# Optimization experiments

Hardware: AMD Instinct MI355X
Metric: run time of the kernel (lower is better)

The kernel has to match this reference:

```python
import jax, jax.numpy as jnp
import numpy as np

B, H, P, K, E, BN = 8, 256, 1024, 32, 4, 64


def setup_inputs() -> dict:
    key = jax.random.key(0)
    ks = jax.random.split(key, 8)
    current = jax.random.normal(ks[0], (B, H, P), dtype=jnp.float32)
    neighbor_features = jax.random.normal(ks[1], (B, H, P, K), dtype=jnp.float32)
    # binary {0,1} validity mask, stored as float like the torch module expects
    neighbor_validity = jax.random.randint(ks[2], (B, 1, P, K), 0, 2).astype(jnp.float32)
    edge_features = jax.random.normal(ks[3], (B, E, P, K), dtype=jnp.float32)
    # 1x1 Conv2d weights flattened to matrices: (out_ch, in_ch)
    w1 = jax.random.normal(ks[4], (BN, 2 * H + E), dtype=jnp.float32) * 0.05
    b1 = jnp.zeros((BN,), dtype=jnp.float32)
    w2 = jax.random.normal(ks[5], (BN,), dtype=jnp.float32) * 0.05  # second conv: out_ch=1
    b2 = jnp.zeros((), dtype=jnp.float32)
    return {
        "current": current,
        "neighbor_features": neighbor_features,
        "neighbor_validity": neighbor_validity,
        "edge_features": edge_features,
        "w1": w1,
        "b1": b1,
        "w2": w2,
        "b2": b2,
    }


def reference(current, neighbor_features, neighbor_validity, edge_features, w1, b1, w2, b2):
    h_dim = current.shape[1]
    # Split the 1x1-conv weight along the concat axis so we never materialize
    # the [B, 2H+E, P, K] concatenated tensor (same math as cat + conv1x1).
    w1c = w1[:, :h_dim]            # acts on broadcast center features
    w1n = w1[:, h_dim:2 * h_dim]   # acts on neighbor features
    w1e = w1[:, 2 * h_dim:]        # acts on edge features

    hid = (
        jnp.einsum("bcp,oc->bop", current, w1c)[:, :, :, None]
        + jnp.einsum("bcpk,oc->bopk", neighbor_features, w1n)
        + jnp.einsum("bcpk,oc->bopk", edge_features, w1e)
        + b1[None, :, None, None]
    )
    hid = jax.nn.relu(hid)                                  # (B, BN, P, K)
    logits = jnp.einsum("bopk,o->bpk", hid, w2) + b2        # (B, P, K)

    valid = neighbor_validity[:, 0] > 0.5                   # (B, P, K) bool
    logits = jnp.where(valid, logits, -jnp.inf)
    has_any = jnp.any(valid, axis=-1, keepdims=True)        # (B, P, 1)
    logits_safe = jnp.where(has_any, logits, 0.0)           # all-masked rows -> 0 logits
    weights = jax.nn.softmax(logits_safe, axis=-1)
    weights = jnp.where(has_any & valid, weights, 0.0)      # zero weight on pads / empty rows

    pooled = jnp.einsum("bcpk,bpk->bcp", neighbor_features, weights)
    return pooled
```

## Files before the change

### kernel.cpp

```cpp
#include <hip/hip_runtime.h>
#include <math.h>


#define B_ 8
#define H_ 256
#define P_ 1024
#define K_ 32
#define E_ 4
#define BN_ 64

typedef __attribute__((ext_vector_type(8))) short short8;
typedef __attribute__((ext_vector_type(4))) float floatx4;

__device__ __forceinline__ unsigned short bf16_rne(float f) {
  unsigned u = __float_as_uint(f);
  u += 0x7fffu + ((u >> 16) & 1u);
  return (unsigned short)(u >> 16);
}
__device__ __forceinline__ unsigned pack_bf16_rne(float lo, float hi) {
  unsigned u0 = __float_as_uint(lo);
  u0 += 0x7fffu + ((u0 >> 16) & 1u);
  unsigned u1 = __float_as_uint(hi);
  u1 += 0x7fffu + ((u1 >> 16) & 1u);
  return (u0 >> 16) | (u1 & 0xffff0000u);
}

__global__ __launch_bounds__(256) void prep_kernel(
    const float* __restrict__ w1, unsigned short* __restrict__ w1m) {
  int i = blockIdx.x * 256 + threadIdx.x;
  if (i >= 4 * 17 * 64 * 8) return;
  int j = i & 7, lane = (i >> 3) & 63;
  int kt = i >> 9;
  int mt = kt / 17, ki = kt % 17;
  int o = mt * 16 + (lane & 15);
  int c = ki * 32 + (lane >> 4) * 8 + j;
  float v = (c < 516) ? w1[o * 516 + c] : 0.f;
  w1m[i] = bf16_rne(v);
}

__global__ __launch_bounds__(256, 4) void soft_attn_agg_kernel(
    const float* __restrict__ cur,
    const float* __restrict__ nf,
    const float* __restrict__ nv,
    const float* __restrict__ ef,
    const unsigned short* __restrict__ w1m,
    const float* __restrict__ b1,
    const float* __restrict__ w2,
    float* __restrict__ out) {
  __shared__ unsigned s_nf_dw[BN_ * 132];
  __shared__ __align__(16) unsigned short s_curb[2][H_];
  __shared__ __align__(16) unsigned short s_edgeT[2][K_][8];
  __shared__ float s_valid[64];
  __shared__ __align__(16) float s_b1[BN_];
  __shared__ __align__(16) float s_w2[BN_];
  __shared__ float s_lg[BN_];
  __shared__ float s_wt[64];

  const int t = threadIdx.x;
  const unsigned bid = blockIdx.x;
  const unsigned xcd = bid & 7u, sidx = bid >> 3;
  const int p0 = (int)(2u * (xcd * 64u + (sidx & 63u)));
  const int b = (int)(sidx >> 6);

  const int w = t >> 6;
  const int lane = t & 63;
  const int q = lane >> 4;
  const int ln15 = lane & 15;

  {
    const int r = lane >> 4, s = lane & 15;
    const float* base = nf + ((size_t)b * H_ * P_ + (size_t)p0) * K_;
    const int X = (s & 14) << 1;
    unsigned* dst0 = s_nf_dw + (4 * s) * 132;
#pragma unroll
    for (int i = 0; i < 8; ++i) {
      const int c_even = w * 64 + i * 8 + 2 * r;
      const float4 fa = *(const float4*)(base + (size_t)c_even * (P_ * K_) + s * 4);
      const float4 fb = *(const float4*)(base + (size_t)(c_even + 1) * (P_ * K_) + s * 4);
      const int cp = (32 * w + 4 * i + r) ^ X;
      unsigned* dst = dst0 + cp;
      dst[0]   = pack_bf16_rne(fa.x, fb.x);
      dst[132] = pack_bf16_rne(fa.y, fb.y);
      dst[264] = pack_bf16_rne(fa.z, fb.z);
      dst[396] = pack_bf16_rne(fa.w, fb.w);
    }
  }
  {
    const float* cp_ = cur + ((size_t)b * H_ + t) * P_ + p0;
    s_curb[0][t] = bf16_rne(cp_[0]);
    s_curb[1][t] = bf16_rne(cp_[1]);
  }
  if (t < 64) {
    s_valid[t] = nv[((size_t)b * P_ + p0) * K_ + t];
    const int pl = t >> 5, k = t & 31;
    const float* ep = ef + (((size_t)b * E_ * P_) + p0 + pl) * K_ + k;
    float e0 = ep[0];
    float e1 = ep[(size_t)P_ * K_];
    float e2 = ep[(size_t)(2 * P_) * K_];
    float e3 = ep[(size_t)(3 * P_) * K_];
    uint4 d;
    d.x = pack_bf16_rne(e0, e1);
    d.y = pack_bf16_rne(e2, e3);
    d.z = 0u; d.w = 0u;
    *(uint4*)&s_edgeT[pl][k][0] = d;
  } else if (t < 128) {
    s_b1[t - 64] = b1[t - 64];
  } else if (t < 192) {
    s_w2[t - 128] = w2[t - 128];
  }
  __syncthreads();

  floatx4 acc[4];
#pragma unroll
  for (int mt = 0; mt < 4; ++mt)
    acc[mt] = *(const floatx4*)&s_b1[mt * 16 + q * 4];

  const int pl_w = w >> 1;
  const int n_lane = 16 * w + ln15;
  const int bxor = ((2 * w + (ln15 >> 3)) & 7) << 2;
  const unsigned* bsrc = s_nf_dw + n_lane * 132;
  const unsigned short* w1m_l = w1m + (size_t)lane * 8;

#pragma unroll
  for (int ki = 0; ki < 17; ++ki) {
    short8 bfrag;
    if (ki < 8) {
      bfrag = *(const short8*)&s_curb[pl_w][ki * 32 + q * 8];
    } else if (ki < 16) {
      bfrag = *(const short8*)(bsrc + ((16 * (ki - 8) + 4 * q) ^ bxor));
    } else {
      bfrag = *(const short8*)&s_edgeT[pl_w][(w & 1) * 16 + ln15][0];
    }
#pragma unroll
    for (int mt = 0; mt < 4; ++mt) {
      short8 a = *(const short8*)(w1m_l + (size_t)(mt * 17 + ki) * 512);
      acc[mt] = __builtin_amdgcn_mfma_f32_16x16x32_bf16(a, bfrag, acc[mt], 0, 0, 0);
    }
  }

  {
    float lp = 0.f;
#pragma unroll
    for (int mt = 0; mt < 4; ++mt) {
      const floatx4 w2v = *(const floatx4*)&s_w2[mt * 16 + q * 4];
#pragma unroll
      for (int r = 0; r < 4; ++r)
        lp = fmaf(fmaxf(acc[mt][r], 0.f), w2v[r], lp);
    }
    lp += __shfl_xor(lp, 16);
    lp += __shfl_xor(lp, 32);
    if (lane < 16) s_lg[16 * w + lane] = lp;
  }
  __syncthreads();

  if (t < 64) {
    float lg = s_lg[t];
    bool v = s_valid[t] > 0.5f;
    float ml = v ? lg : -INFINITY;
#pragma unroll
    for (int m = 1; m < 32; m <<= 1) ml = fmaxf(ml, __shfl_xor(ml, m));
    float e = v ? __expf(lg - ml) : 0.f;
    float ssum = e;
#pragma unroll
    for (int m = 1; m < 32; m <<= 1) ssum += __shfl_xor(ssum, m);
    s_wt[t] = (ml > -INFINITY) ? (e / ssum) : 0.f;
  }
  __syncthreads();

  {
    const int pl = t >> 7, cpair = t & 127;
    float acc0 = 0.f, acc1 = 0.f;
#pragma unroll
    for (int k = 0; k < K_; ++k) {
      const int n = pl * 32 + k;
      const int xr = ((n >> 3) & 7) << 2;
      const unsigned u = s_nf_dw[n * 132 + (cpair ^ xr)];
      const float wtk = s_wt[n];
      acc0 = fmaf(__uint_as_float(u << 16), wtk, acc0);
      acc1 = fmaf(__uint_as_float(u & 0xffff0000u), wtk, acc1);
    }
    float* op = out + ((size_t)b * H_ + 2 * cpair) * P_ + p0 + pl;
    op[0] = acc0;
    op[P_] = acc1;
  }
}

extern "C" void kernel_launch(void* const* d_in, const int* in_sizes, int n_in,
                              void* d_out, int out_size, void* d_ws,
                              size_t ws_size, hipStream_t stream) {
  const float* cur = (const float*)d_in[0];
  const float* nf  = (const float*)d_in[1];
  const float* nv  = (const float*)d_in[2];
  const float* ef  = (const float*)d_in[3];
  const float* w1  = (const float*)d_in[4];
  const float* b1  = (const float*)d_in[5];
  const float* w2  = (const float*)d_in[6];

  unsigned short* w1m = (unsigned short*)d_ws;
  prep_kernel<<<(4 * 17 * 64 * 8 + 255) / 256, 256, 0, stream>>>(w1, w1m);
  soft_attn_agg_kernel<<<B_ * P_ / 2, 256, 0, stream>>>(
      cur, nf, nv, ef, w1m, b1, w2, (float*)d_out);
}
```

Before: 417.5 us.

## Process eight points per 512-thread block with coalesced neighbor loads

Each block now covers eight points with eight waves instead of two points with four waves. Neighbor features are staged by having each thread read one contiguous neighbor element across many channels, which gives coalesced global loads, and the XOR swizzle in shared memory is dropped. Each wave computes two neighbor tiles for one point, so every weight fragment feeds two MFMAs, and the output is written as float2. The shared-memory footprint grows to about 135KB, so only one block fits per CU, which reduces latency hiding, and the unswizzled layout may cause more LDS bank conflicts.

```diff
diff --git a/kernel.cpp b/kernel.cpp
--- a/kernel.cpp
+++ b/kernel.cpp
@@ -38,7 +38,7 @@
   w1m[i] = bf16_rne(v);
 }
 
-__global__ __launch_bounds__(256, 4) void soft_attn_agg_kernel(
+__global__ __launch_bounds__(512, 2) void soft_attn_agg_kernel(
     const float* __restrict__ cur,
     const float* __restrict__ nf,
     const float* __restrict__ nv,
@@ -47,20 +47,21 @@
     const float* __restrict__ b1,
     const float* __restrict__ w2,
     float* __restrict__ out) {
-  __shared__ unsigned s_nf_dw[BN_ * 132];
-  __shared__ __align__(16) unsigned short s_curb[2][H_];
-  __shared__ __align__(16) unsigned short s_edgeT[2][K_][8];
-  __shared__ float s_valid[64];
-  __shared__ __align__(16) float s_b1[BN_];
-  __shared__ __align__(16) float s_w2[BN_];
-  __shared__ float s_lg[BN_];
-  __shared__ float s_wt[64];
+  __shared__ unsigned s_nf[256 * 132];
+  __shared__ unsigned short s_curb[8][264];
+  __shared__ unsigned s_edge[8][32][4];
+  __shared__ float s_valid[256];
+  __shared__ float s_b1v[BN_];
+  __shared__ float s_w2v[BN_];
+  __shared__ float s_lg[256];
+  __shared__ float s_wt[256];
 
   const int t = threadIdx.x;
   const unsigned bid = blockIdx.x;
-  const unsigned xcd = bid & 7u, sidx = bid >> 3;
-  const int p0 = (int)(2u * (xcd * 64u + (sidx & 63u)));
-  const int b = (int)(sidx >> 6);
+  const unsigned xcd = bid & 7u, sx = bid >> 3;
+  const int b = (int)(sx >> 4);
+  const int pg = (int)(xcd * 16u + (sx & 15u));
+  const int p0 = pg * 8;
 
   const int w = t >> 6;
   const int lane = t & 63;
@@ -68,92 +69,120 @@
   const int ln15 = lane & 15;
 
   {
-    const int r = lane >> 4, s = lane & 15;
-    const float* base = nf + ((size_t)b * H_ * P_ + (size_t)p0) * K_;
-    const int X = (s & 14) << 1;
-    unsigned* dst0 = s_nf_dw + (4 * s) * 132;
-#pragma unroll
-    for (int i = 0; i < 8; ++i) {
-      const int c_even = w * 64 + i * 8 + 2 * r;
-      const float4 fa = *(const float4*)(base + (size_t)c_even * (P_ * K_) + s * 4);
-      const float4 fb = *(const float4*)(base + (size_t)(c_even + 1) * (P_ * K_) + s * 4);
-      const int cp = (32 * w + 4 * i + r) ^ X;
-      unsigned* dst = dst0 + cp;
-      dst[0]   = pack_bf16_rne(fa.x, fb.x);
-      dst[132] = pack_bf16_rne(fa.y, fb.y);
-      dst[264] = pack_bf16_rne(fa.z, fb.z);
-      dst[396] = pack_bf16_rne(fa.w, fb.w);
-    }
-  }
-  {
-    const float* cp_ = cur + ((size_t)b * H_ + t) * P_ + p0;
-    s_curb[0][t] = bf16_rne(cp_[0]);
-    s_curb[1][t] = bf16_rne(cp_[1]);
-  }
-  if (t < 64) {
+    const int n = t & 255, ch = t >> 8;
+    const float* gp = nf + (size_t)b * (H_ * P_ * K_) +
+                      (size_t)(ch * 128) * (P_ * K_) + (size_t)p0 * K_ + n;
+    unsigned* drow = s_nf + n * 132 + ch * 64;
+#pragma unroll 4
+    for (int i = 0; i < 16; ++i) {
+      const float* gc = gp + (size_t)(8 * i) * (P_ * K_);
+      float f0 = gc[0];
+      float f1 = gc[(size_t)(P_ * K_)];
+      float f2 = gc[(size_t)(2 * P_ * K_)];
+      float f3 = gc[(size_t)(3 * P_ * K_)];
+      float f4 = gc[(size_t)(4 * P_ * K_)];
+      float f5 = gc[(size_t)(5 * P_ * K_)];
+      float f6 = gc[(size_t)(6 * P_ * K_)];
+      float f7 = gc[(size_t)(7 * P_ * K_)];
+      uint4 d;
+      d.x = pack_bf16_rne(f0, f1);
+      d.y = pack_bf16_rne(f2, f3);
+      d.z = pack_bf16_rne(f4, f5);
+      d.w = pack_bf16_rne(f6, f7);
+      *(uint4*)&drow[4 * i] = d;
+    }
+  }
+  if (t < 256) {
+    const float* cb = cur + ((size_t)b * H_ + t) * P_ + p0;
+    float4 ca = *(const float4*)cb;
+    float4 cc = *(const float4*)(cb + 4);
+    s_curb[0][t] = bf16_rne(ca.x);
+    s_curb[1][t] = bf16_rne(ca.y);
+    s_curb[2][t] = bf16_rne(ca.z);
+    s_curb[3][t] = bf16_rne(ca.w);
+    s_curb[4][t] = bf16_rne(cc.x);
+    s_curb[5][t] = bf16_rne(cc.y);
+    s_curb[6][t] = bf16_rne(cc.z);
+    s_curb[7][t] = bf16_rne(cc.w);
     s_valid[t] = nv[((size_t)b * P_ + p0) * K_ + t];
     const int pl = t >> 5, k = t & 31;
-    const float* ep = ef + (((size_t)b * E_ * P_) + p0 + pl) * K_ + k;
+    const float* ep = ef + (size_t)b * (E_ * P_ * K_) + (size_t)p0 * K_ + t;
     float e0 = ep[0];
-    float e1 = ep[(size_t)P_ * K_];
-    float e2 = ep[(size_t)(2 * P_) * K_];
-    float e3 = ep[(size_t)(3 * P_) * K_];
+    float e1 = ep[(size_t)(P_ * K_)];
+    float e2 = ep[(size_t)(2 * P_ * K_)];
+    float e3 = ep[(size_t)(3 * P_ * K_)];
     uint4 d;
     d.x = pack_bf16_rne(e0, e1);
     d.y = pack_bf16_rne(e2, e3);
-    d.z = 0u; d.w = 0u;
-    *(uint4*)&s_edgeT[pl][k][0] = d;
-  } else if (t < 128) {
-    s_b1[t - 64] = b1[t - 64];
-  } else if (t < 192) {
-    s_w2[t - 128] = w2[t - 128];
+    d.z = 0u;
+    d.w = 0u;
+    *(uint4*)&s_edge[pl][k][0] = d;
+  } else if (t < 320) {
+    s_b1v[t - 256] = b1[t - 256];
+  } else if (t < 384) {
+    s_w2v[t - 320] = w2[t - 320];
   }
   __syncthreads();
 
-  floatx4 acc[4];
-#pragma unroll
-  for (int mt = 0; mt < 4; ++mt)
-    acc[mt] = *(const floatx4*)&s_b1[mt * 16 + q * 4];
-
-  const int pl_w = w >> 1;
-  const int n_lane = 16 * w + ln15;
-  const int bxor = ((2 * w + (ln15 >> 3)) & 7) << 2;
-  const unsigned* bsrc = s_nf_dw + n_lane * 132;
+  floatx4 acc[4][2];
+#pragma unroll
+  for (int mt = 0; mt < 4; ++mt) {
+    floatx4 binit = *(const floatx4*)&s_b1v[mt * 16 + q * 4];
+    acc[mt][0] = binit;
+    acc[mt][1] = binit;
+  }
   const unsigned short* w1m_l = w1m + (size_t)lane * 8;
-
-#pragma unroll
-  for (int ki = 0; ki < 17; ++ki) {
-    short8 bfrag;
-    if (ki < 8) {
-      bfrag = *(const short8*)&s_curb[pl_w][ki * 32 + q * 8];
-    } else if (ki < 16) {
-      bfrag = *(const short8*)(bsrc + ((16 * (ki - 8) + 4 * q) ^ bxor));
-    } else {
-      bfrag = *(const short8*)&s_edgeT[pl_w][(w & 1) * 16 + ln15][0];
-    }
+  const int pl_w = w;
+
+#pragma unroll
+  for (int ki = 0; ki < 8; ++ki) {
+    short8 bc = *(const short8*)&s_curb[pl_w][ki * 32 + q * 8];
 #pragma unroll
     for (int mt = 0; mt < 4; ++mt) {
       short8 a = *(const short8*)(w1m_l + (size_t)(mt * 17 + ki) * 512);
-      acc[mt] = __builtin_amdgcn_mfma_f32_16x16x32_bf16(a, bfrag, acc[mt], 0, 0, 0);
-    }
-  }
-
+      acc[mt][0] = __builtin_amdgcn_mfma_f32_16x16x32_bf16(a, bc, acc[mt][0], 0, 0, 0);
+      acc[mt][1] = __builtin_amdgcn_mfma_f32_16x16x32_bf16(a, bc, acc[mt][1], 0, 0, 0);
+    }
+  }
+#pragma unroll
+  for (int ck = 0; ck < 8; ++ck) {
+    short8 bn0 = *(const short8*)(s_nf + ((2 * w) * 16 + ln15) * 132 + 16 * ck + 4 * q);
+    short8 bn1 = *(const short8*)(s_nf + ((2 * w + 1) * 16 + ln15) * 132 + 16 * ck + 4 * q);
+#pragma unroll
+    for (int mt = 0; mt < 4; ++mt) {
+      short8 a = *(const short8*)(w1m_l + (size_t)(mt * 17 + 8 + ck) * 512);
+      acc[mt][0] = __builtin_amdgcn_mfma_f32_16x16x32_bf16(a, bn0, acc[mt][0], 0, 0, 0);
+      acc[mt][1] = __builtin_amdgcn_mfma_f32_16x16x32_bf16(a, bn1, acc[mt][1], 0, 0, 0);
+    }
+  }
   {
+    short8 be0 = *(const short8*)&s_edge[pl_w][ln15][0];
+    short8 be1 = *(const short8*)&s_edge[pl_w][16 + ln15][0];
+#pragma unroll
+    for (int mt = 0; mt < 4; ++mt) {
+      short8 a = *(const short8*)(w1m_l + (size_t)(mt * 17 + 16) * 512);
+      acc[mt][0] = __builtin_amdgcn_mfma_f32_16x16x32_bf16(a, be0, acc[mt][0], 0, 0, 0);
+      acc[mt][1] = __builtin_amdgcn_mfma_f32_16x16x32_bf16(a, be1, acc[mt][1], 0, 0, 0);
+    }
+  }
+
+#pragma unroll
+  for (int nti = 0; nti < 2; ++nti) {
     float lp = 0.f;
 #pragma unroll
     for (int mt = 0; mt < 4; ++mt) {
-      const floatx4 w2v = *(const floatx4*)&s_w2[mt * 16 + q * 4];
+      const floatx4 w2v = *(const floatx4*)&s_w2v[mt * 16 + q * 4];
 #pragma unroll
       for (int r = 0; r < 4; ++r)
-        lp = fmaf(fmaxf(acc[mt][r], 0.f), w2v[r], lp);
+        lp = fmaf(fmaxf(acc[mt][nti][r], 0.f), w2v[r], lp);
     }
     lp += __shfl_xor(lp, 16);
     lp += __shfl_xor(lp, 32);
-    if (lane < 16) s_lg[16 * w + lane] = lp;
+    if (lane < 16) s_lg[(2 * w + nti) * 16 + ln15] = lp;
   }
   __syncthreads();
 
-  if (t < 64) {
+  if (t < 256) {
     float lg = s_lg[t];
     bool v = s_valid[t] > 0.5f;
     float ml = v ? lg : -INFINITY;
@@ -168,20 +197,25 @@
   __syncthreads();
 
   {
-    const int pl = t >> 7, cpair = t & 127;
-    float acc0 = 0.f, acc1 = 0.f;
+    const int cpr = t & 127, ph = t >> 7;
+    const int nb = ph * 64;
+    float a0e = 0.f, a0o = 0.f, a1e = 0.f, a1o = 0.f;
 #pragma unroll
     for (int k = 0; k < K_; ++k) {
-      const int n = pl * 32 + k;
-      const int xr = ((n >> 3) & 7) << 2;
-      const unsigned u = s_nf_dw[n * 132 + (cpair ^ xr)];
-      const float wtk = s_wt[n];
-      acc0 = fmaf(__uint_as_float(u << 16), wtk, acc0);
-      acc1 = fmaf(__uint_as_float(u & 0xffff0000u), wtk, acc1);
-    }
-    float* op = out + ((size_t)b * H_ + 2 * cpair) * P_ + p0 + pl;
-    op[0] = acc0;
-    op[P_] = acc1;
+      const unsigned u0 = s_nf[(nb + k) * 132 + cpr];
+      const unsigned u1 = s_nf[(nb + 32 + k) * 132 + cpr];
+      const float wt0 = s_wt[nb + k];
+      const float wt1 = s_wt[nb + 32 + k];
+      a0e = fmaf(__uint_as_float(u0 << 16), wt0, a0e);
+      a0o = fmaf(__uint_as_float(u0 & 0xffff0000u), wt0, a0o);
+      a1e = fmaf(__uint_as_float(u1 << 16), wt1, a1e);
+      a1o = fmaf(__uint_as_float(u1 & 0xffff0000u), wt1, a1o);
+    }
+    float* op = out + ((size_t)b * H_ + 2 * cpr) * P_ + p0 + 2 * ph;
+    float2 ve; ve.x = a0e; ve.y = a1e;
+    float2 vo; vo.x = a0o; vo.y = a1o;
+    *(float2*)op = ve;
+    *(float2*)(op + P_) = vo;
   }
 }
 
@@ -198,6 +232,6 @@
 
   unsigned short* w1m = (unsigned short*)d_ws;
   prep_kernel<<<(4 * 17 * 64 * 8 + 255) / 256, 256, 0, stream>>>(w1, w1m);
-  soft_attn_agg_kernel<<<B_ * P_ / 2, 256, 0, stream>>>(
+  soft_attn_agg_kernel<<<B_ * P_ / 8, 512, 0, stream>>>(
       cur, nf, nv, ef, w1m, b1, w2, (float*)d_out);
 }
```

Measured after the change: 408.1 us. -2.2%, faster.
